# Kernel tuning notes

Measured on AMD Instinct MI355X. Metric: run time of the kernel, lower is better.

## Reference

```python
import jax, jax.numpy as jnp
import numpy as np
from jax import lax

EPS = 1e-5
SLOPE = 0.2

def knn_idx(x, k):
    # x: [B, C, N] -> neighbor indices [B, N, k] (largest negative sq-dist, self included)
    inner = jnp.einsum('bcn,bcm->bnm', x, x)          # [B,N,N]
    xx = jnp.sum(x * x, axis=1)                        # [B,N]
    pair = 2.0 * inner - xx[:, :, None] - xx[:, None, :]
    return lax.top_k(pair, k)[1]                       # [B,N,k]

def graph_feature(x, idx):
    # x: [B,C,N], idx: [B,N,k] -> edge features [B,N,k,2C] = (x_j - x_i, x_i)
    feat = jnp.transpose(x, (0, 2, 1))                 # [B,N,C]
    nbr = jax.vmap(lambda f, i: f[i])(feat, idx)       # [B,N,k,C]
    ctr = jnp.broadcast_to(feat[:, :, None, :], nbr.shape)
    return jnp.concatenate([nbr - ctr, ctr], axis=-1)  # [B,N,k,2C]

def bn(x, gamma, beta, axes):
    mu = jnp.mean(x, axis=axes, keepdims=True)
    var = jnp.var(x, axis=axes, keepdims=True)
    return (x - mu) * lax.rsqrt(var + EPS) * gamma + beta

def edge_conv(e, w, gamma, beta):
    # e: [B,N,k,2C], w: [O,2C] (1x1 conv, no bias) -> [B,N,O] after BN+LeakyReLU+max over k
    h = jnp.einsum('bnkc,oc->bnko', e, w)
    h = jax.nn.leaky_relu(bn(h, gamma, beta, (0, 1, 2)), SLOPE)
    return jnp.max(h, axis=2)                          # [B,N,O]

def setup_inputs() -> dict:
    key = jax.random.key(0)
    ks = jax.random.split(key, 8)
    B, C, N, O = 8, 3, 4096, 64
    x = jax.random.normal(ks[0], (B, C, N), jnp.float32)
    w_s = jax.random.normal(ks[1], (O, 2 * C), jnp.float32) * (1.0 / np.sqrt(2 * C))
    w_l = jax.random.normal(ks[2], (O, 2 * C), jnp.float32) * (1.0 / np.sqrt(2 * C))
    w_f = jax.random.normal(ks[3], (O, 2 * O), jnp.float32) * (1.0 / np.sqrt(2 * O))
    g_s = jnp.ones((O,)); b_s = jnp.zeros((O,))
    g_l = jnp.ones((O,)); b_l = jnp.zeros((O,))
    g_f = jnp.ones((O,)); b_f = jnp.zeros((O,))
    return {"x": x, "w_s": w_s, "g_s": g_s, "b_s": b_s,
            "w_l": w_l, "g_l": g_l, "b_l": b_l,
            "w_f": w_f, "g_f": g_f, "b_f": b_f}

def reference(x, w_s, g_s, b_s, w_l, g_l, b_l, w_f, g_f, b_f):
    K_SMALL, K_LARGE = 20, 40
    idx_s = knn_idx(x, K_SMALL)
    idx_l = knn_idx(x, K_LARGE)
    h_s = edge_conv(graph_feature(x, idx_s), w_s, g_s, b_s)   # [B,N,O]
    h_l = edge_conv(graph_feature(x, idx_l), w_l, g_l, b_l)   # [B,N,O]
    h = jnp.concatenate([h_s, h_l], axis=-1)                  # [B,N,2O]
    h = jnp.einsum('bnc,oc->bno', h, w_f)                     # fuse 1x1 conv
    h = jax.nn.leaky_relu(bn(h, g_f, b_f, (0, 1)), SLOPE)
    return jnp.transpose(h, (0, 2, 1))                        # [B,O,N]
```

## Files before the change

kernel.cpp:

```cpp
#include <hip/hip_runtime.h>

#define B_ 8
#define N_ 4096
#define O_ 64
#define KL 40
#define KS 20
#define EPSV 1e-5
#define SLOPE 0.2f

typedef unsigned long long u64;
typedef unsigned int u32;

__device__ __forceinline__ float leaky(float v) { return v >= 0.f ? v : SLOPE * v; }

__device__ __forceinline__ u32 mfloat(float x) {
    const u32 u = __float_as_uint(x);
    return (u & 0x80000000u) ? ~u : (u | 0x80000000u);
}
__device__ __forceinline__ float unmfloat(u32 m) {
    return __uint_as_float((m & 0x80000000u) ? (m ^ 0x80000000u) : ~m);
}

template <int S>
__device__ __forceinline__ u64 xor_ex64(u64 v, int dsaddr) {
    if constexpr (S == 1 || S == 2 || S == 8) {
        constexpr int CTRL = (S == 1) ? 0xB1 : (S == 2) ? 0x4E : 0x128;
        const int lo = __builtin_amdgcn_update_dpp(0, (int)(u32)v, CTRL, 0xF, 0xF, true);
        const int hi = __builtin_amdgcn_update_dpp(0, (int)(u32)(v >> 32), CTRL, 0xF, 0xF, true);
        return ((u64)(u32)hi << 32) | (u32)lo;
    } else {
        const int lo = __builtin_amdgcn_ds_bpermute(dsaddr, (int)(u32)v);
        const int hi = __builtin_amdgcn_ds_bpermute(dsaddr, (int)(u32)(v >> 32));
        return ((u64)(u32)hi << 32) | (u32)lo;
    }
}

template <int K, int S>
__device__ __forceinline__ void stage_pair(u64& a, u64& e, int lane, int dsaddr) {
    const u64 oa = xor_ex64<S>(a, dsaddr);
    const u64 oe = xor_ex64<S>(e, dsaddr);
    const bool sel = (((lane & K) == 0) == ((lane & S) == 0));
    a = ((a < oa) == sel) ? a : oa;
    e = ((e < oe) == sel) ? e : oe;
}

__device__ __forceinline__ void sort64_pair(u64& a, u64& e, int lane,
                                            int a4, int a16, int a32) {
    stage_pair<2, 1>(a, e, lane, 0);
    stage_pair<4, 2>(a, e, lane, 0);    stage_pair<4, 1>(a, e, lane, 0);
    stage_pair<8, 4>(a, e, lane, a4);   stage_pair<8, 2>(a, e, lane, 0);    stage_pair<8, 1>(a, e, lane, 0);
    stage_pair<16, 8>(a, e, lane, 0);   stage_pair<16, 4>(a, e, lane, a4);  stage_pair<16, 2>(a, e, lane, 0);   stage_pair<16, 1>(a, e, lane, 0);
    stage_pair<32, 16>(a, e, lane, a16); stage_pair<32, 8>(a, e, lane, 0);  stage_pair<32, 4>(a, e, lane, a4);  stage_pair<32, 2>(a, e, lane, 0);  stage_pair<32, 1>(a, e, lane, 0);
    stage_pair<64, 32>(a, e, lane, a32); stage_pair<64, 16>(a, e, lane, a16); stage_pair<64, 8>(a, e, lane, 0); stage_pair<64, 4>(a, e, lane, a4); stage_pair<64, 2>(a, e, lane, 0); stage_pair<64, 1>(a, e, lane, 0);
}

__device__ __forceinline__ void merge_pair(u64& L0, u64& L1, u64 a, u64 e, int lane,
                                           int a4, int a16, int a32, int a63) {
    const u64 ra = xor_ex64<63>(a, a63);
    const u64 re = xor_ex64<63>(e, a63);
    L0 = (L0 < ra) ? L0 : ra;
    L1 = (L1 < re) ? L1 : re;
    stage_pair<0, 32>(L0, L1, lane, a32);
    stage_pair<0, 16>(L0, L1, lane, a16);
    stage_pair<0, 8>(L0, L1, lane, 0);
    stage_pair<0, 4>(L0, L1, lane, a4);
    stage_pair<0, 2>(L0, L1, lane, 0);
    stage_pair<0, 1>(L0, L1, lane, 0);
}

__global__ __launch_bounds__(1024) void bucket_kernel(const float* __restrict__ x,
                                                      float4* __restrict__ sxp,
                                                      int* __restrict__ perm,
                                                      float2* __restrict__ cb,
                                                      float4* __restrict__ xo4) {
    __shared__ int hist[256];
    __shared__ int ofs[256];
    __shared__ u32 xsm[4096];
    __shared__ float redmin[16], redmax[16];
    __shared__ u32 wmin[64], wmax[64];
    const int b = blockIdx.x;
    const float* xb = x + (size_t)b * 3 * N_;
    const int t = threadIdx.x;
    float xv[4];
    float mn = INFINITY, mx = -INFINITY;
#pragma unroll
    for (int p = 0; p < 4; ++p) {
        xv[p] = xb[t + p * 1024];
        mn = fminf(mn, xv[p]); mx = fmaxf(mx, xv[p]);
    }
#pragma unroll
    for (int s = 1; s < 64; s <<= 1) {
        mn = fminf(mn, __shfl_xor(mn, s));
        mx = fmaxf(mx, __shfl_xor(mx, s));
    }
    if ((t & 63) == 0) { redmin[t >> 6] = mn; redmax[t >> 6] = mx; }
    if (t < 256) hist[t] = 0;
    __syncthreads();
    if (t == 0) {
        float m0 = INFINITY, m1 = -INFINITY;
        for (int w = 0; w < 16; ++w) { m0 = fminf(m0, redmin[w]); m1 = fmaxf(m1, redmax[w]); }
        redmin[0] = m0; redmax[0] = m1;
    }
    __syncthreads();
    const float xmin = redmin[0];
    const float scale = 256.0f / fmaxf(redmax[0] - xmin, 1e-20f);
    int bk[4];
#pragma unroll
    for (int p = 0; p < 4; ++p) {
        bk[p] = min(255, max(0, (int)((xv[p] - xmin) * scale)));
        atomicAdd(&hist[bk[p]], 1);
    }
    __syncthreads();
    if (t == 0) {
        int acc = 0;
        for (int k = 0; k < 256; ++k) { ofs[k] = acc; acc += hist[k]; }
    }
    if (t < 64) { wmin[t] = 0xFFFFFFFFu; wmax[t] = 0; }
    __syncthreads();
#pragma unroll
    for (int p = 0; p < 4; ++p) {
        const int i = t + p * 1024;
        const int dst = atomicAdd(&ofs[bk[p]], 1);
        const float cx = xv[p], cy = xb[N_ + i], cz = xb[2 * N_ + i];
        sxp[((size_t)b << 12) + dst] = make_float4(2.f * cx, 2.f * cy, 2.f * cz,
                                                   -(cx * cx + cy * cy + cz * cz));
        perm[(b << 12) + dst] = i;
        xo4[((size_t)b << 12) + i] = make_float4(cx, cy, cz, 0.f);
        xsm[dst] = mfloat(cx);
    }
    __syncthreads();
#pragma unroll
    for (int p = 0; p < 4; ++p) {
        const int pos = t + p * 1024;
        const int w = pos >> 6;
        atomicMin(&wmin[w], xsm[pos]);
        atomicMax(&wmax[w], xsm[pos]);
    }
    __syncthreads();
    if (t == 0) {
        u32 sm = 0xFFFFFFFFu;
        for (int w = 63; w >= 0; --w) { sm = min(sm, wmin[w]); wmin[w] = sm; }
        u32 pm2 = 0;
        for (int w = 0; w < 64; ++w) { pm2 = max(pm2, wmax[w]); wmax[w] = pm2; }
    }
    __syncthreads();
    if (t < 64) cb[(b << 6) + t] = make_float2(unmfloat(wmin[t]), unmfloat(wmax[t]));
}

__global__ __launch_bounds__(256, 8) void knn_kernel(const float4* __restrict__ sxp,
                                                     const int* __restrict__ perm,
                                                     const float2* __restrict__ cb,
                                                     const float4* __restrict__ xo4,
                                                     const float* __restrict__ w_s,
                                                     const float* __restrict__ w_l,
                                                     float* __restrict__ max_s,
                                                     float* __restrict__ min_s,
                                                     float* __restrict__ max_l,
                                                     float* __restrict__ min_l,
                                                     float* __restrict__ qstats) {
    __shared__ u64 buf[4][2][128];
    __shared__ float2 cbl[64];
    const int sbid = ((blockIdx.x & 7) << 9) | (blockIdx.x >> 3);
    const int b = sbid >> 9;
    const int qbase = (sbid & 511) << 3;
    const int tid = threadIdx.x;
    const int wave = tid >> 6, lane = tid & 63;
    if (tid < 64) cbl[tid] = cb[(b << 6) + tid];
    const int a4 = (lane ^ 4) << 2, a16 = (lane ^ 16) << 2;
    const int a32 = (lane ^ 32) << 2, a63 = (lane ^ 63) << 2;
    const float4* sp = sxp + ((size_t)b << 12);
    const int* pm = perm + (b << 12);
    const float4* xo = xo4 + ((size_t)b << 12);
    const int i0 = qbase + wave * 2;
    const float4 p0 = sp[i0], p1 = sp[i0 + 1];
    const float qx0 = 0.5f * p0.x, qy0 = 0.5f * p0.y, qz0 = 0.5f * p0.z, nw0 = p0.w;
    const float qx1 = 0.5f * p1.x, qy1 = 0.5f * p1.y, qz1 = 0.5f * p1.z, nw1 = p1.w;
    const float qxmin = fminf(qx0, qx1), qxmax = fmaxf(qx0, qx1);
    u64 L0 = ~0ull, L1 = ~0ull;
    float th0 = -INFINITY, th1 = -INFINITY;
    int cnt0 = 0, cnt1 = 0;
    __syncthreads();
    const int home = i0 >> 6;
    int cl = home - 1, cr = home + 1;
    bool openL = (cl >= 0), openR = (cr < 64);
    bool takeR = true;
    int c = home;
    float4 cd = sp[(c << 6) + lane];
    int pj = pm[(c << 6) + lane];
    for (;;) {
        int cn = -1;
        for (;;) {
            if (!openL && !openR) break;
            const bool pickR = openR && (takeR || !openL);
            takeR = !pickR;
            const float r2 = -fminf(th0, th1);
            if (pickR) {
                const float dx = cbl[cr].x - qxmax;
                if (dx > 0.f && dx * dx > r2) { openR = false; continue; }
                cn = cr++; if (cr >= 64) openR = false; break;
            } else {
                const float dx = qxmin - cbl[cl].y;
                if (dx > 0.f && dx * dx > r2) { openL = false; continue; }
                cn = cl--; if (cl < 0) openL = false; break;
            }
        }
        float4 nd = make_float4(0.f, 0.f, 0.f, 0.f);
        int nj = 0;
        if (cn >= 0) { nd = sp[(cn << 6) + lane]; nj = pm[(cn << 6) + lane]; }
        {
            const float d0 = fmaf(qx0, cd.x, fmaf(qy0, cd.y, fmaf(qz0, cd.z, cd.w + nw0)));
            const float d1 = fmaf(qx1, cd.x, fmaf(qy1, cd.y, fmaf(qz1, cd.z, cd.w + nw1)));
            const bool pr0 = (d0 >= th0), pr1 = (d1 >= th1);
            const u64 m0 = __ballot(pr0), m1 = __ballot(pr1);
            if (m0) {
                const int pos = cnt0 + __builtin_amdgcn_mbcnt_hi(
                    (u32)(m0 >> 32), __builtin_amdgcn_mbcnt_lo((u32)m0, 0));
                if (pr0) {
                    const u32 kd = __float_as_uint(fminf(d0, -0.0f));
                    buf[wave][0][pos] = ((u64)kd << 32) | (u32)pj;
                }
                cnt0 += __popcll(m0);
            }
            if (m1) {
                const int pos = cnt1 + __builtin_amdgcn_mbcnt_hi(
                    (u32)(m1 >> 32), __builtin_amdgcn_mbcnt_lo((u32)m1, 0));
                if (pr1) {
                    const u32 kd = __float_as_uint(fminf(d1, -0.0f));
                    buf[wave][1][pos] = ((u64)kd << 32) | (u32)pj;
                }
                cnt1 += __popcll(m1);
            }
            if ((cnt0 | cnt1) >= 64) {
                const int t0 = min(cnt0, 64), t1 = min(cnt1, 64);
                u64 a = (lane < t0) ? buf[wave][0][cnt0 - t0 + lane] : ~0ull;
                u64 e = (lane < t1) ? buf[wave][1][cnt1 - t1 + lane] : ~0ull;
                sort64_pair(a, e, lane, a4, a16, a32);
                merge_pair(L0, L1, a, e, lane, a4, a16, a32, a63);
                th0 = __uint_as_float((u32)__builtin_amdgcn_readlane((int)(u32)(L0 >> 32), KL - 1));
                th1 = __uint_as_float((u32)__builtin_amdgcn_readlane((int)(u32)(L1 >> 32), KL - 1));
                cnt0 -= t0; cnt1 -= t1;
            }
        }
        if (cn < 0) break;
        cd = nd; pj = nj; c = cn;
    }
    if ((cnt0 | cnt1) > 0) {
        u64 a = (lane < cnt0) ? buf[wave][0][lane] : ~0ull;
        u64 e = (lane < cnt1) ? buf[wave][1][lane] : ~0ull;
        sort64_pair(a, e, lane, a4, a16, a32);
        merge_pair(L0, L1, a, e, lane, a4, a16, a32, a63);
    }
    const int lw = lane * 6;
    const float ws0 = w_s[lw], ws1 = w_s[lw + 1], ws2 = w_s[lw + 2];
    const float ds0 = w_s[lw + 3] - ws0, ds1 = w_s[lw + 4] - ws1, ds2 = w_s[lw + 5] - ws2;
    const float wl0 = w_l[lw], wl1 = w_l[lw + 1], wl2 = w_l[lw + 2];
    const float dl0 = w_l[lw + 3] - wl0, dl1 = w_l[lw + 4] - wl1, dl2 = w_l[lw + 5] - wl2;
    const int oi0 = pm[i0], oi1 = pm[i0 + 1];
#pragma unroll
    for (int q = 0; q < 2; ++q) {
        const float qx = q ? qx1 : qx0, qy = q ? qy1 : qy0, qz = q ? qz1 : qz0;
        const int Llo = q ? (int)(u32)L1 : (int)(u32)L0;
        const int oi = q ? oi1 : oi0;
        const float cs = ds0 * qx + ds1 * qy + ds2 * qz;
        const float cq = dl0 * qx + dl1 * qy + dl2 * qz;
        float mxs = -INFINITY, mns = INFINITY, mxl = -INFINITY, mnl = INFINITY;
        float sums = 0.f, sss = 0.f, suml = 0.f, ssl = 0.f;
#pragma unroll 8
        for (int k = 0; k < KL; ++k) {
            const int j = __builtin_amdgcn_readlane(Llo, k);
            const float4 xj = xo[j];
            const float hl = fmaf(wl0, xj.x, fmaf(wl1, xj.y, wl2 * xj.z)) + cq;
            mxl = fmaxf(mxl, hl); mnl = fminf(mnl, hl);
            suml += hl; ssl = fmaf(hl, hl, ssl);
            if (k < KS) {
                const float hs = fmaf(ws0, xj.x, fmaf(ws1, xj.y, ws2 * xj.z)) + cs;
                mxs = fmaxf(mxs, hs); mns = fminf(mns, hs);
                sums += hs; sss = fmaf(hs, hs, sss);
            }
        }
        const size_t base = (size_t)((b << 12) + oi) * 64 + lane;
        max_s[base] = mxs; min_s[base] = mns;
        max_l[base] = mxl; min_l[base] = mnl;
        float* qs = qstats + (size_t)((b << 12) + oi) * 256;
        qs[lane] = sums; qs[64 + lane] = sss;
        qs[128 + lane] = suml; qs[192 + lane] = ssl;
    }
}

__global__ void reduce1a_kernel(const float* __restrict__ qstats, double* __restrict__ partialD1) {
    const int t = threadIdx.x;
    double acc = 0.0;
    const int r0 = blockIdx.x * 256;
    for (int r = 0; r < 256; ++r) acc += (double)qstats[(size_t)(r0 + r) * 256 + t];
    partialD1[(size_t)blockIdx.x * 256 + t] = acc;
}

__global__ void reduce1b_kernel(const double* __restrict__ partialD1,
                                const float* __restrict__ g_s, const float* __restrict__ b_s,
                                const float* __restrict__ g_l, const float* __restrict__ b_l,
                                float* __restrict__ sb1) {
    const int t = threadIdx.x;
    double acc = 0.0;
    for (int r = 0; r < 128; ++r) acc += partialD1[(size_t)r * 256 + t];
    __shared__ double sums[256];
    sums[t] = acc;
    __syncthreads();
    if (t < 64) {
        const double ns = (double)B_ * N_ * KS;
        const double nl = (double)B_ * N_ * KL;
        double mu = sums[t] / ns;
        double var = sums[64 + t] / ns - mu * mu;
        double sc = (double)g_s[t] / sqrt(var + EPSV);
        sb1[t] = (float)sc;
        sb1[64 + t] = (float)((double)b_s[t] - mu * sc);
        mu = sums[128 + t] / nl;
        var = sums[192 + t] / nl - mu * mu;
        sc = (double)g_l[t] / sqrt(var + EPSV);
        sb1[128 + t] = (float)sc;
        sb1[192 + t] = (float)((double)b_l[t] - mu * sc);
    }
}

__global__ __launch_bounds__(256) void fuse_kernel(
    const float* __restrict__ max_s, const float* __restrict__ min_s,
    const float* __restrict__ max_l, const float* __restrict__ min_l,
    const float* __restrict__ sb1, const float* __restrict__ w_f,
    float* __restrict__ f_buf, float* __restrict__ partial2) {
    __shared__ float wfT[128 * 64];
    __shared__ float av[4][128];
    __shared__ float red[2][4][64];
    const int tid = threadIdx.x;
    for (int t = tid; t < 8192; t += 256) {
        const int c = t >> 6, o = t & 63;
        wfT[t] = w_f[o * 128 + c];
    }
    const int sbid = ((blockIdx.x & 7) << 8) + (blockIdx.x >> 3);
    const int wave = tid >> 6, lane = tid & 63;
    const float sc_s = sb1[lane], bi_s = sb1[64 + lane];
    const float sc_l = sb1[128 + lane], bi_l = sb1[192 + lane];
    float sum_f = 0.f, ss_f = 0.f;
    __syncthreads();
    for (int p = 0; p < 4; ++p) {
        const int bn = (sbid * 4 + wave) * 4 + p;
        const size_t base = (size_t)bn * 64 + lane;
        const float hs = sc_s >= 0.f ? max_s[base] : min_s[base];
        const float a_s = leaky(fmaf(sc_s, hs, bi_s));
        const float hl = sc_l >= 0.f ? max_l[base] : min_l[base];
        const float a_l = leaky(fmaf(sc_l, hl, bi_l));
        av[wave][lane] = a_s;
        av[wave][64 + lane] = a_l;
        float acc = 0.f;
#pragma unroll
        for (int c = 0; c < 128; ++c) acc = fmaf(wfT[c * 64 + lane], av[wave][c], acc);
        f_buf[base] = acc;
        sum_f += acc;
        ss_f = fmaf(acc, acc, ss_f);
    }
    red[0][wave][lane] = sum_f;
    red[1][wave][lane] = ss_f;
    __syncthreads();
    if (tid < 128) {
        const int st = tid >> 6, o = tid & 63;
        partial2[(size_t)blockIdx.x * 128 + tid] =
            red[st][0][o] + red[st][1][o] + red[st][2][o] + red[st][3][o];
    }
}

__global__ void reduce2a_kernel(const float* __restrict__ partial2, double* __restrict__ partialD2) {
    const int t = threadIdx.x;
    double acc = 0.0;
    const int r0 = blockIdx.x * 32;
    for (int r = 0; r < 32; ++r) acc += (double)partial2[(size_t)(r0 + r) * 128 + t];
    partialD2[(size_t)blockIdx.x * 128 + t] = acc;
}

__global__ void reduce2b_kernel(const double* __restrict__ partialD2,
                                const float* __restrict__ g_f, const float* __restrict__ b_f,
                                float* __restrict__ sb2) {
    const int t = threadIdx.x;
    double acc = 0.0;
    for (int r = 0; r < 64; ++r) acc += partialD2[(size_t)r * 128 + t];
    __shared__ double sums[128];
    sums[t] = acc;
    __syncthreads();
    if (t < 64) {
        const double n = (double)B_ * N_;
        const double mu = sums[t] / n;
        const double var = sums[64 + t] / n - mu * mu;
        const double sc = (double)g_f[t] / sqrt(var + EPSV);
        sb2[t] = (float)sc;
        sb2[64 + t] = (float)((double)b_f[t] - mu * sc);
    }
}

__global__ __launch_bounds__(256) void final_kernel(const float* __restrict__ f_buf,
                                                    const float* __restrict__ sb2,
                                                    float* __restrict__ out) {
    __shared__ float tile[64][65];
    const int sbid = ((blockIdx.x & 7) << 6) + (blockIdx.x >> 3);
    const int b = sbid >> 6;
    const int n0 = (sbid & 63) << 6;
#pragma unroll
    for (int r = 0; r < 16; ++r) {
        const int t = r * 256 + threadIdx.x;
        const int n = t >> 6, o = t & 63;
        const float v = f_buf[(size_t)((b << 12) + n0 + n) * 64 + o];
        const float h = fmaf(sb2[o], v, sb2[64 + o]);
        tile[n][o] = leaky(h);
    }
    __syncthreads();
#pragma unroll
    for (int r = 0; r < 16; ++r) {
        const int t = r * 256 + threadIdx.x;
        const int o = t >> 6, n = t & 63;
        out[(size_t)((b << 6) + o) * N_ + n0 + n] = tile[n][o];
    }
}

extern "C" void kernel_launch(void* const* d_in, const int* in_sizes, int n_in,
                              void* d_out, int out_size, void* d_ws, size_t ws_size,
                              hipStream_t stream) {
    (void)in_sizes; (void)n_in; (void)out_size; (void)ws_size;
    const float* x   = (const float*)d_in[0];
    const float* w_s = (const float*)d_in[1];
    const float* g_s = (const float*)d_in[2];
    const float* b_s = (const float*)d_in[3];
    const float* w_l = (const float*)d_in[4];
    const float* g_l = (const float*)d_in[5];
    const float* b_l = (const float*)d_in[6];
    const float* w_f = (const float*)d_in[7];
    const float* g_f = (const float*)d_in[8];
    const float* b_f = (const float*)d_in[9];
    float* out = (float*)d_out;
    char* ws = (char*)d_ws;

    constexpr size_t SZ_PT   = (size_t)B_ * N_ * 64 * 4;
    constexpr size_t OFF_MXS = 0;
    constexpr size_t OFF_MNS = OFF_MXS + SZ_PT;
    constexpr size_t OFF_MXL = OFF_MNS + SZ_PT;
    constexpr size_t OFF_MNL = OFF_MXL + SZ_PT;
    constexpr size_t OFF_QST = OFF_MNL + SZ_PT;
    constexpr size_t OFF_PD1 = OFF_QST + (size_t)B_ * N_ * 256 * 4;
    constexpr size_t OFF_SB1 = OFF_PD1 + (size_t)128 * 256 * 8;
    constexpr size_t OFF_F   = OFF_SB1 + 1024;
    constexpr size_t OFF_P2  = OFF_F + SZ_PT;
    constexpr size_t OFF_PD2 = OFF_P2 + (size_t)2048 * 128 * 4;
    constexpr size_t OFF_SB2 = OFF_PD2 + (size_t)64 * 128 * 8;
    constexpr size_t OFF_SXP = OFF_SB2 + 1024;
    constexpr size_t OFF_PRM = OFF_SXP + (size_t)B_ * N_ * 16;
    constexpr size_t OFF_CB  = OFF_PRM + (size_t)B_ * N_ * 4;
    constexpr size_t OFF_XO4 = OFF_CB + (size_t)B_ * 64 * 8;

    float*  mxs  = (float*)(ws + OFF_MXS);
    float*  mns  = (float*)(ws + OFF_MNS);
    float*  mxl  = (float*)(ws + OFF_MXL);
    float*  mnl  = (float*)(ws + OFF_MNL);
    float*  qst  = (float*)(ws + OFF_QST);
    double* pd1  = (double*)(ws + OFF_PD1);
    float*  sb1  = (float*)(ws + OFF_SB1);
    float*  fb   = (float*)(ws + OFF_F);
    float*  p2   = (float*)(ws + OFF_P2);
    double* pd2  = (double*)(ws + OFF_PD2);
    float*  sb2  = (float*)(ws + OFF_SB2);
    float4* sxp  = (float4*)(ws + OFF_SXP);
    int*    prm  = (int*)(ws + OFF_PRM);
    float2* cbv  = (float2*)(ws + OFF_CB);
    float4* xo4  = (float4*)(ws + OFF_XO4);

    hipLaunchKernelGGL(bucket_kernel, dim3(8), dim3(1024), 0, stream, x, sxp, prm, cbv, xo4);
    hipLaunchKernelGGL(knn_kernel, dim3(4096), dim3(256), 0, stream,
                       sxp, prm, cbv, xo4, w_s, w_l, mxs, mns, mxl, mnl, qst);
    hipLaunchKernelGGL(reduce1a_kernel, dim3(128), dim3(256), 0, stream, qst, pd1);
    hipLaunchKernelGGL(reduce1b_kernel, dim3(1), dim3(256), 0, stream, pd1, g_s, b_s, g_l, b_l, sb1);
    hipLaunchKernelGGL(fuse_kernel, dim3(2048), dim3(256), 0, stream,
                       mxs, mns, mxl, mnl, sb1, w_f, fb, p2);
    hipLaunchKernelGGL(reduce2a_kernel, dim3(64), dim3(128), 0, stream, p2, pd2);
    hipLaunchKernelGGL(reduce2b_kernel, dim3(1), dim3(128), 0, stream, pd2, g_f, b_f, sb2);
    hipLaunchKernelGGL(final_kernel, dim3(512), dim3(256), 0, stream, fb, sb2, out);
}
```

Baseline: 224.7 us.

## Make bucket sort deterministic, preload neighbor coords, block-reduce stats, merge reduce2

The bucket kernel replaces shared-memory atomic histogram and offset scattering with per-wave rank counting and a column scan. This makes the point permutation deterministic and removes atomic contention. The window min/max uses a per-thread loop instead of atomics. The knn kernel loads each lane's neighbor coordinates once and broadcasts them with readlane, replacing 40 serial dependent gathers. It also reduces BN statistics inside each block so the qstats buffer and the reduce1a pass shrink. The two-stage reduce2 is merged into one 1024-thread kernel, which saves a launch but puts the whole reduction on a single block.

```diff
diff --git a/kernel.cpp b/kernel.cpp
--- a/kernel.cpp
+++ b/kernel.cpp
@@ -10,6 +10,7 @@
 
 typedef unsigned long long u64;
 typedef unsigned int u32;
+typedef unsigned short u16;
 
 __device__ __forceinline__ float leaky(float v) { return v >= 0.f ? v : SLOPE * v; }
 
@@ -73,14 +74,16 @@
                                                       int* __restrict__ perm,
                                                       float2* __restrict__ cb,
                                                       float4* __restrict__ xo4) {
-    __shared__ int hist[256];
-    __shared__ int ofs[256];
+    __shared__ u16 cnt16[64][256];
+    __shared__ int base[256];
     __shared__ u32 xsm[4096];
     __shared__ float redmin[16], redmax[16];
     __shared__ u32 wmin[64], wmax[64];
+    __shared__ u16 bkb[16][64];
     const int b = blockIdx.x;
     const float* xb = x + (size_t)b * 3 * N_;
     const int t = threadIdx.x;
+    const int wave = t >> 6, lane = t & 63;
     float xv[4];
     float mn = INFINITY, mx = -INFINITY;
 #pragma unroll
@@ -93,8 +96,11 @@
         mn = fminf(mn, __shfl_xor(mn, s));
         mx = fmaxf(mx, __shfl_xor(mx, s));
     }
-    if ((t & 63) == 0) { redmin[t >> 6] = mn; redmax[t >> 6] = mx; }
-    if (t < 256) hist[t] = 0;
+    if (lane == 0) { redmin[wave] = mn; redmax[wave] = mx; }
+    {
+        u32* cz = (u32*)&cnt16[0][0];
+        for (int i = t; i < 64 * 128; i += 1024) cz[i] = 0;
+    }
     __syncthreads();
     if (t == 0) {
         float m0 = INFINITY, m1 = -INFINITY;
@@ -104,23 +110,44 @@
     __syncthreads();
     const float xmin = redmin[0];
     const float scale = 256.0f / fmaxf(redmax[0] - xmin, 1e-20f);
-    int bk[4];
+    int bk[4], rk[4];
 #pragma unroll
     for (int p = 0; p < 4; ++p) {
         bk[p] = min(255, max(0, (int)((xv[p] - xmin) * scale)));
-        atomicAdd(&hist[bk[p]], 1);
+        const int c = p * 16 + wave;
+        bkb[wave][lane] = (u16)bk[p];
+        __builtin_amdgcn_wave_barrier();
+        int r = 0, later = 0;
+        for (int l = 0; l < 64; ++l) {
+            const int eq = (bkb[wave][l] == (u16)bk[p]);
+            r += eq & (l < lane);
+            later += eq & (l > lane);
+        }
+        rk[p] = r;
+        if (later == 0) cnt16[c][bk[p]] = (u16)(r + 1);
+        __builtin_amdgcn_wave_barrier();
+    }
+    __syncthreads();
+    if (t < 256) {
+        int acc = 0;
+        for (int c = 0; c < 64; ++c) {
+            const int tmp = cnt16[c][t];
+            cnt16[c][t] = (u16)acc;
+            acc += tmp;
+        }
+        base[t] = acc;
     }
     __syncthreads();
     if (t == 0) {
         int acc = 0;
-        for (int k = 0; k < 256; ++k) { ofs[k] = acc; acc += hist[k]; }
-    }
-    if (t < 64) { wmin[t] = 0xFFFFFFFFu; wmax[t] = 0; }
+        for (int k = 0; k < 256; ++k) { const int tmp = base[k]; base[k] = acc; acc += tmp; }
+    }
     __syncthreads();
 #pragma unroll
     for (int p = 0; p < 4; ++p) {
         const int i = t + p * 1024;
-        const int dst = atomicAdd(&ofs[bk[p]], 1);
+        const int c = p * 16 + wave;
+        const int dst = base[bk[p]] + (int)cnt16[c][bk[p]] + rk[p];
         const float cx = xv[p], cy = xb[N_ + i], cz = xb[2 * N_ + i];
         sxp[((size_t)b << 12) + dst] = make_float4(2.f * cx, 2.f * cy, 2.f * cz,
                                                    -(cx * cx + cy * cy + cz * cz));
@@ -129,12 +156,13 @@
         xsm[dst] = mfloat(cx);
     }
     __syncthreads();
-#pragma unroll
-    for (int p = 0; p < 4; ++p) {
-        const int pos = t + p * 1024;
-        const int w = pos >> 6;
-        atomicMin(&wmin[w], xsm[pos]);
-        atomicMax(&wmax[w], xsm[pos]);
+    if (t < 64) {
+        u32 lo = 0xFFFFFFFFu, hi = 0;
+        for (int l = 0; l < 64; ++l) {
+            const u32 v = xsm[(t << 6) + l];
+            lo = min(lo, v); hi = max(hi, v);
+        }
+        wmin[t] = lo; wmax[t] = hi;
     }
     __syncthreads();
     if (t == 0) {
@@ -160,6 +188,7 @@
                                                      float* __restrict__ qstats) {
     __shared__ u64 buf[4][2][128];
     __shared__ float2 cbl[64];
+    __shared__ float sred[4][4][64];
     const int sbid = ((blockIdx.x & 7) << 9) | (blockIdx.x >> 3);
     const int b = sbid >> 9;
     const int qbase = (sbid & 511) << 3;
@@ -256,24 +285,28 @@
     const float wl0 = w_l[lw], wl1 = w_l[lw + 1], wl2 = w_l[lw + 2];
     const float dl0 = w_l[lw + 3] - wl0, dl1 = w_l[lw + 4] - wl1, dl2 = w_l[lw + 5] - wl2;
     const int oi0 = pm[i0], oi1 = pm[i0 + 1];
+    const float4 n0v = xo[(int)(u32)L0 & 4095];
+    const float4 n1v = xo[(int)(u32)L1 & 4095];
+    float stat[4][2];
 #pragma unroll
     for (int q = 0; q < 2; ++q) {
         const float qx = q ? qx1 : qx0, qy = q ? qy1 : qy0, qz = q ? qz1 : qz0;
-        const int Llo = q ? (int)(u32)L1 : (int)(u32)L0;
+        const float nx = q ? n1v.x : n0v.x, ny = q ? n1v.y : n0v.y, nz = q ? n1v.z : n0v.z;
         const int oi = q ? oi1 : oi0;
         const float cs = ds0 * qx + ds1 * qy + ds2 * qz;
         const float cq = dl0 * qx + dl1 * qy + dl2 * qz;
         float mxs = -INFINITY, mns = INFINITY, mxl = -INFINITY, mnl = INFINITY;
         float sums = 0.f, sss = 0.f, suml = 0.f, ssl = 0.f;
-#pragma unroll 8
+#pragma unroll
         for (int k = 0; k < KL; ++k) {
-            const int j = __builtin_amdgcn_readlane(Llo, k);
-            const float4 xj = xo[j];
-            const float hl = fmaf(wl0, xj.x, fmaf(wl1, xj.y, wl2 * xj.z)) + cq;
+            const float sx = __uint_as_float((u32)__builtin_amdgcn_readlane(__float_as_uint(nx), k));
+            const float sy = __uint_as_float((u32)__builtin_amdgcn_readlane(__float_as_uint(ny), k));
+            const float sz = __uint_as_float((u32)__builtin_amdgcn_readlane(__float_as_uint(nz), k));
+            const float hl = fmaf(wl0, sx, fmaf(wl1, sy, wl2 * sz)) + cq;
             mxl = fmaxf(mxl, hl); mnl = fminf(mnl, hl);
             suml += hl; ssl = fmaf(hl, hl, ssl);
             if (k < KS) {
-                const float hs = fmaf(ws0, xj.x, fmaf(ws1, xj.y, ws2 * xj.z)) + cs;
+                const float hs = fmaf(ws0, sx, fmaf(ws1, sy, ws2 * sz)) + cs;
                 mxs = fmaxf(mxs, hs); mns = fminf(mns, hs);
                 sums += hs; sss = fmaf(hs, hs, sss);
             }
@@ -281,17 +314,23 @@
         const size_t base = (size_t)((b << 12) + oi) * 64 + lane;
         max_s[base] = mxs; min_s[base] = mns;
         max_l[base] = mxl; min_l[base] = mnl;
-        float* qs = qstats + (size_t)((b << 12) + oi) * 256;
-        qs[lane] = sums; qs[64 + lane] = sss;
-        qs[128 + lane] = suml; qs[192 + lane] = ssl;
+        stat[0][q] = sums; stat[1][q] = sss; stat[2][q] = suml; stat[3][q] = ssl;
+    }
+#pragma unroll
+    for (int s = 0; s < 4; ++s) sred[wave][s][lane] = stat[s][0] + stat[s][1];
+    __syncthreads();
+    if (tid < 256) {
+        const int st = tid >> 6, ch = tid & 63;
+        qstats[(size_t)blockIdx.x * 256 + tid] =
+            sred[0][st][ch] + sred[1][st][ch] + sred[2][st][ch] + sred[3][st][ch];
     }
 }
 
 __global__ void reduce1a_kernel(const float* __restrict__ qstats, double* __restrict__ partialD1) {
     const int t = threadIdx.x;
     double acc = 0.0;
-    const int r0 = blockIdx.x * 256;
-    for (int r = 0; r < 256; ++r) acc += (double)qstats[(size_t)(r0 + r) * 256 + t];
+    const int r0 = blockIdx.x * 128;
+    for (int r = 0; r < 128; ++r) acc += (double)qstats[(size_t)(r0 + r) * 256 + t];
     partialD1[(size_t)blockIdx.x * 256 + t] = acc;
 }
 
@@ -301,7 +340,7 @@
                                 float* __restrict__ sb1) {
     const int t = threadIdx.x;
     double acc = 0.0;
-    for (int r = 0; r < 128; ++r) acc += partialD1[(size_t)r * 256 + t];
+    for (int r = 0; r < 32; ++r) acc += partialD1[(size_t)r * 256 + t];
     __shared__ double sums[256];
     sums[t] = acc;
     __syncthreads();
@@ -366,27 +405,29 @@
     }
 }
 
-__global__ void reduce2a_kernel(const float* __restrict__ partial2, double* __restrict__ partialD2) {
+__global__ __launch_bounds__(1024) void reduce2_kernel(const float* __restrict__ partial2,
+                                                       const float* __restrict__ g_f,
+                                                       const float* __restrict__ b_f,
+                                                       float* __restrict__ sb2) {
+    __shared__ double seg[8][128];
+    __shared__ double tot[128];
     const int t = threadIdx.x;
+    const int col = t & 127, sg = t >> 7;
     double acc = 0.0;
-    const int r0 = blockIdx.x * 32;
-    for (int r = 0; r < 32; ++r) acc += (double)partial2[(size_t)(r0 + r) * 128 + t];
-    partialD2[(size_t)blockIdx.x * 128 + t] = acc;
-}
-
-__global__ void reduce2b_kernel(const double* __restrict__ partialD2,
-                                const float* __restrict__ g_f, const float* __restrict__ b_f,
-                                float* __restrict__ sb2) {
-    const int t = threadIdx.x;
-    double acc = 0.0;
-    for (int r = 0; r < 64; ++r) acc += partialD2[(size_t)r * 128 + t];
-    __shared__ double sums[128];
-    sums[t] = acc;
+    const int r0 = sg * 256;
+    for (int r = 0; r < 256; ++r) acc += (double)partial2[(size_t)(r0 + r) * 128 + col];
+    seg[sg][col] = acc;
+    __syncthreads();
+    if (t < 128) {
+        double s = 0.0;
+        for (int g = 0; g < 8; ++g) s += seg[g][t];
+        tot[t] = s;
+    }
     __syncthreads();
     if (t < 64) {
         const double n = (double)B_ * N_;
-        const double mu = sums[t] / n;
-        const double var = sums[64 + t] / n - mu * mu;
+        const double mu = tot[t] / n;
+        const double var = tot[64 + t] / n - mu * mu;
         const double sc = (double)g_f[t] / sqrt(var + EPSV);
         sb2[t] = (float)sc;
         sb2[64 + t] = (float)((double)b_f[t] - mu * sc);
@@ -440,12 +481,11 @@
     constexpr size_t OFF_MXL = OFF_MNS + SZ_PT;
     constexpr size_t OFF_MNL = OFF_MXL + SZ_PT;
     constexpr size_t OFF_QST = OFF_MNL + SZ_PT;
-    constexpr size_t OFF_PD1 = OFF_QST + (size_t)B_ * N_ * 256 * 4;
-    constexpr size_t OFF_SB1 = OFF_PD1 + (size_t)128 * 256 * 8;
+    constexpr size_t OFF_PD1 = OFF_QST + (size_t)4096 * 256 * 4;
+    constexpr size_t OFF_SB1 = OFF_PD1 + (size_t)32 * 256 * 8;
     constexpr size_t OFF_F   = OFF_SB1 + 1024;
     constexpr size_t OFF_P2  = OFF_F + SZ_PT;
-    constexpr size_t OFF_PD2 = OFF_P2 + (size_t)2048 * 128 * 4;
-    constexpr size_t OFF_SB2 = OFF_PD2 + (size_t)64 * 128 * 8;
+    constexpr size_t OFF_SB2 = OFF_P2 + (size_t)2048 * 128 * 4;
     constexpr size_t OFF_SXP = OFF_SB2 + 1024;
     constexpr size_t OFF_PRM = OFF_SXP + (size_t)B_ * N_ * 16;
     constexpr size_t OFF_CB  = OFF_PRM + (size_t)B_ * N_ * 4;
@@ -460,7 +500,6 @@
     float*  sb1  = (float*)(ws + OFF_SB1);
     float*  fb   = (float*)(ws + OFF_F);
     float*  p2   = (float*)(ws + OFF_P2);
-    double* pd2  = (double*)(ws + OFF_PD2);
     float*  sb2  = (float*)(ws + OFF_SB2);
     float4* sxp  = (float4*)(ws + OFF_SXP);
     int*    prm  = (int*)(ws + OFF_PRM);
@@ -470,11 +509,10 @@
     hipLaunchKernelGGL(bucket_kernel, dim3(8), dim3(1024), 0, stream, x, sxp, prm, cbv, xo4);
     hipLaunchKernelGGL(knn_kernel, dim3(4096), dim3(256), 0, stream,
                        sxp, prm, cbv, xo4, w_s, w_l, mxs, mns, mxl, mnl, qst);
-    hipLaunchKernelGGL(reduce1a_kernel, dim3(128), dim3(256), 0, stream, qst, pd1);
+    hipLaunchKernelGGL(reduce1a_kernel, dim3(32), dim3(256), 0, stream, qst, pd1);
     hipLaunchKernelGGL(reduce1b_kernel, dim3(1), dim3(256), 0, stream, pd1, g_s, b_s, g_l, b_l, sb1);
     hipLaunchKernelGGL(fuse_kernel, dim3(2048), dim3(256), 0, stream,
                        mxs, mns, mxl, mnl, sb1, w_f, fb, p2);
-    hipLaunchKernelGGL(reduce2a_kernel, dim3(64), dim3(128), 0, stream, p2, pd2);
-    hipLaunchKernelGGL(reduce2b_kernel, dim3(1), dim3(128), 0, stream, pd2, g_f, b_f, sb2);
+    hipLaunchKernelGGL(reduce2_kernel, dim3(1), dim3(1024), 0, stream, p2, g_f, b_f, sb2);
     hipLaunchKernelGGL(final_kernel, dim3(512), dim3(256), 0, stream, fb, sb2, out);
 }
```

After: 232.6 us. +3.5%, slower.
